# Kernel tuning notes

Measured on AMD Instinct MI355X. Metric: run time of the kernel, lower is better.

Reference implementation:

```python
import jax, jax.numpy as jnp
import numpy as np

B = 16
H_DIM = 512
N_HEADS = 8
HEAD_DIM = H_DIM // N_HEADS  # 64
EPS = 1e-5
DST_LENS = 256 + 16 * np.arange(B)  # ragged dst sizes, total 6016
SRC_LENS = 512 - 8 * np.arange(B)   # ragged src sizes, total 7232


def _pad_info(lens):
    # gather/scatter indices to move between flat ragged layout and [B, Lmax, D]
    lens = np.asarray(lens)
    off = np.concatenate([[0], np.cumsum(lens)[:-1]])
    gid = np.repeat(np.arange(len(lens)), lens)
    pos = np.arange(int(lens.sum())) - np.repeat(off, lens)
    Lmax = int(lens.max())
    mask = jnp.asarray(np.arange(Lmax)[None, :] < lens[:, None])
    return gid, pos, Lmax, mask


def _bn(x, g, b):
    # BatchNorm1d forward with batch statistics (training-mode normalization)
    m = x.mean(0)
    v = ((x - m) ** 2).mean(0)
    return (x - m) / jnp.sqrt(v + EPS) * g + b


def setup_inputs() -> dict:
    key = jax.random.key(0)
    ks = jax.random.split(key, 20)
    total_src = int(SRC_LENS.sum())
    total_dst = int(DST_LENS.sum())
    w = lambda k, shape: jax.random.normal(k, shape, jnp.float32) * 0.02
    return {
        "src_h": jax.random.normal(ks[0], (total_src, H_DIM), jnp.float32),
        "dst_h": jax.random.normal(ks[1], (total_dst, H_DIM), jnp.float32),
        "src_num_verts": jnp.asarray(SRC_LENS, jnp.int32),
        "dst_num_verts": jnp.asarray(DST_LENS, jnp.int32),
        "Wq": w(ks[2], (H_DIM, H_DIM)), "bq": w(ks[3], (H_DIM,)),
        "Wk": w(ks[4], (H_DIM, H_DIM)), "bk": w(ks[5], (H_DIM,)),
        "Wv": w(ks[6], (H_DIM, H_DIM)), "bv": w(ks[7], (H_DIM,)),
        "Wm": w(ks[8], (H_DIM, H_DIM)), "bm": w(ks[9], (H_DIM,)),
        "W1": w(ks[10], (H_DIM, 2 * H_DIM)), "b1": w(ks[11], (H_DIM,)),
        "g1": jnp.ones((H_DIM,), jnp.float32), "be1": jnp.zeros((H_DIM,), jnp.float32),
        "W2": w(ks[12], (H_DIM, H_DIM)), "b2": w(ks[13], (H_DIM,)),
        "g2": jnp.ones((H_DIM,), jnp.float32), "be2": jnp.zeros((H_DIM,), jnp.float32),
    }


def reference(src_h, dst_h, src_num_verts, dst_num_verts,
              Wq, bq, Wk, bk, Wv, bv, Wm, bm,
              W1, b1, g1, be1, W2, b2, g2, be2):
    s_lens = np.asarray(src_num_verts)
    d_lens = np.asarray(dst_num_verts)
    sg, sp, Ls, smask = _pad_info(s_lens)
    dg, dp, Ld, dmask = _pad_info(d_lens)

    # ragged -> padded [B, L, D]
    src_pad = jnp.zeros((B, Ls, H_DIM), src_h.dtype).at[sg, sp].set(src_h)
    dst_pad = jnp.zeros((B, Ld, H_DIM), dst_h.dtype).at[dg, dp].set(dst_h)

    # Conv1d(k=1) projections; channel c = d*num_heads + h -> reshape (head_dim, n_heads)
    q = (dst_pad @ Wq.T + bq).reshape(B, Ld, HEAD_DIM, N_HEADS)
    k = (src_pad @ Wk.T + bk).reshape(B, Ls, HEAD_DIM, N_HEADS)
    v = (src_pad @ Wv.T + bv).reshape(B, Ls, HEAD_DIM, N_HEADS)

    scores = jnp.einsum('bndh,bmdh->bhnm', q, k) / 8.0  # sqrt(head_dim)=8
    scores = jnp.where(smask[:, None, None, :], scores, -1e9)
    attn = jax.nn.softmax(scores, axis=-1)
    o = jnp.einsum('bhnm,bmdh->bndh', attn, v).reshape(B, Ld, H_DIM)
    o = o @ Wm.T + bm  # merge Conv1d(k=1)

    # padded -> ragged
    h_msg = o[dg, dp]  # [total_dst, h_dim]

    h = dst_h
    x = jnp.concatenate([h, h_msg], axis=-1)
    x = _bn(x @ W1.T + b1, g1, be1)
    x = jax.nn.relu(x)
    x = _bn(x @ W2.T + b2, g2, be2)
    return h + x
```

## Files before the change

### kernel.cpp

```cpp
#include <hip/hip_runtime.h>
#include <hip/hip_bf16.h>

#define H_DIM 512
#define N_HEADS 8
#define HEAD_DIM 64
#define NBATCH 16

typedef __attribute__((ext_vector_type(8))) short short8;
typedef __attribute__((ext_vector_type(4))) float floatx4;

typedef unsigned short us16;

#define SW3(r) ((((r) >> 1) & 3) | (((r) & 1) << 2))

#define PERMC(c) ((((c) & 7) << 6) | ((c) >> 3))
#define IPERMC(cp) ((((cp) & 63) << 3) | ((cp) >> 6))

__device__ inline unsigned short f2bf(float f) {
  unsigned int u = __float_as_uint(f);
  unsigned int r = (u + 0x7fffu + ((u >> 16) & 1u)) >> 16;
  return (unsigned short)r;
}

__device__ inline void gld16(const us16* g, us16* l) {
  __builtin_amdgcn_global_load_lds(
      (const __attribute__((address_space(1))) void*)g,
      (__attribute__((address_space(3))) void*)l, 16, 0, 0);
}

__global__ __launch_bounds__(256) void prep_all(
    const float* __restrict__ src_h, const float* __restrict__ dst_h,
    const float* __restrict__ Wq, const float* __restrict__ Wk,
    const float* __restrict__ Wv, const float* __restrict__ W1,
    const float* __restrict__ W2, const float* __restrict__ Wm,
    const float* __restrict__ b1, const float* __restrict__ bm,
    us16* __restrict__ src_bf, us16* __restrict__ dst_bf,
    us16* __restrict__ Wqb, us16* __restrict__ Wkv, us16* __restrict__ Wf,
    us16* __restrict__ W2b, float* __restrict__ b1p, float* __restrict__ st,
    int n_src, int n_dst) {
  __shared__ __align__(16) us16 As[64 * 48];
  __shared__ __align__(16) us16 Bs[64 * 48];
  const int blk = blockIdx.x;
  const int t = threadIdx.x;

  if (blk < 2048) {
    if (blk == 0) {
      float4 z = make_float4(0.f, 0.f, 0.f, 0.f);
      ((float4*)st)[t] = z;
      ((float4*)st)[t + 256] = z;
    }
    const float* srcs[7] = {src_h, dst_h, Wq, Wk, Wv, W1, W2};
    us16* dsts[7] = {src_bf, dst_bf, Wqb, Wkv, Wkv + 262144, Wf, W2b};
    int ns[7] = {n_src, n_dst, 262144, 262144, 262144, 262144, 262144};
    const int md_[7] = {0, 0, 2, 2, 0, 1, 0};
    for (int rg = 0; rg < 7; ++rg) {
      const float* sp = srcs[rg];
      us16* dp = dsts[rg];
      const int mode = md_[rg];
      for (int i = (blk * 256 + t) * 4; i < ns[rg]; i += 2048 * 256 * 4) {
        int js, jd;
        if (mode == 1) {
          js = ((i >> 9) * 1024) + (i & 511);
          jd = js;
        } else if (mode == 2) {
          int r = i >> 9;
          js = i;
          jd = (PERMC(r) << 9) + (i & 511);
        } else {
          js = i; jd = i;
        }
        float4 v = *(const float4*)(sp + js);
        ushort4 o;
        o.x = f2bf(v.x); o.y = f2bf(v.y); o.z = f2bf(v.z); o.w = f2bf(v.w);
        *(ushort4*)(dp + jd) = o;
      }
    }
  } else if (blk < 2112) {
    const int bx = (blk - 2048) & 7, byk = (blk - 2048) >> 3;
    const int w = t >> 6, lane = t & 63;
    const int lane15 = lane & 15, quad = lane >> 4;
    const int wm = w >> 1, wn = w & 1;
    const int bn_ = bx * 64, bk = byk * 64;
    floatx4 acc[2][2];
#pragma unroll
    for (int a = 0; a < 2; ++a)
#pragma unroll
      for (int c = 0; c < 2; ++c) acc[a][c] = (floatx4){0.f, 0.f, 0.f, 0.f};
    for (int j0 = 0; j0 < 512; j0 += 32) {
      {
        int n = t >> 2, jj0 = (t & 3) * 8;
        const float* rp = W1 + (size_t)(bn_ + n) * 1024 + 512 + j0 + jj0;
        float4 va = *(const float4*)(rp);
        float4 vb = *(const float4*)(rp + 4);
        ushort4 pa, pb;
        pa.x = f2bf(va.x); pa.y = f2bf(va.y); pa.z = f2bf(va.z); pa.w = f2bf(va.w);
        pb.x = f2bf(vb.x); pb.y = f2bf(vb.y); pb.z = f2bf(vb.z); pb.w = f2bf(vb.w);
        *(ushort4*)(As + n * 48 + jj0) = pa;
        *(ushort4*)(As + n * 48 + jj0 + 4) = pb;
      }
      {
        int jj = t >> 3, kc0 = (t & 7) * 8;
        const float* rp = Wm + (size_t)(j0 + jj) * 512 + bk + kc0;
        float4 va = *(const float4*)(rp);
        float4 vb = *(const float4*)(rp + 4);
        float vv[8] = {va.x, va.y, va.z, va.w, vb.x, vb.y, vb.z, vb.w};
#pragma unroll
        for (int e = 0; e < 8; ++e) Bs[(kc0 + e) * 48 + jj] = f2bf(vv[e]);
      }
      __syncthreads();
      short8 a_[2], b_[2];
#pragma unroll
      for (int mt = 0; mt < 2; ++mt)
        a_[mt] = *(const short8*)(As + (wm * 32 + mt * 16 + lane15) * 48 + quad * 8);
#pragma unroll
      for (int nt = 0; nt < 2; ++nt)
        b_[nt] = *(const short8*)(Bs + (wn * 32 + nt * 16 + lane15) * 48 + quad * 8);
#pragma unroll
      for (int mt = 0; mt < 2; ++mt)
#pragma unroll
        for (int nt = 0; nt < 2; ++nt)
          acc[mt][nt] = __builtin_amdgcn_mfma_f32_16x16x32_bf16(
              a_[mt], b_[nt], acc[mt][nt], 0, 0, 0);
      __syncthreads();
    }
#pragma unroll
    for (int mt = 0; mt < 2; ++mt) {
      int n0 = bn_ + wm * 32 + mt * 16 + quad * 4;
#pragma unroll
      for (int nt = 0; nt < 2; ++nt) {
        int k = bk + wn * 32 + nt * 16 + lane15;
        int kp = PERMC(k);
#pragma unroll
        for (int r = 0; r < 4; ++r)
          Wf[(size_t)(n0 + r) * 1024 + 512 + kp] = f2bf(acc[mt][nt][r]);
      }
    }
  } else {
    int n = (blk - 2112) * 256 + t;
    if (n < 512) {
      const float* rp = W1 + (size_t)n * 1024 + 512;
      float s = 0.f;
      for (int j = 0; j < 512; j += 4) {
        float4 a = *(const float4*)(rp + j);
        float4 c = *(const float4*)(bm + j);
        s += a.x * c.x + a.y * c.y + a.z * c.z + a.w * c.w;
      }
      b1p[n] = b1[n] + s;
    }
  }
}

__device__ inline void gemm_body(
    const us16* __restrict__ A1, const us16* __restrict__ A2,
    const us16* __restrict__ W,
    const float* __restrict__ bias0, const float* __restrict__ bias1,
    void* __restrict__ C0, void* __restrict__ C1, float* __restrict__ stats,
    int M, int N, int K, int mode, int bx, int by) {
  __shared__ __align__(16) us16 As[2 * 64 * 64];
  __shared__ __align__(16) us16 Bs[2 * 128 * 64];
  const int t = threadIdx.x, w = t >> 6, lane = t & 63;
  const int lane15 = lane & 15, quad = lane >> 4;
  const int bm = bx * 64, bn = by * 128;
  const int lrow = lane >> 3;
  const int sl = lane & 7;

  floatx4 acc[4][2];
#pragma unroll
  for (int a = 0; a < 4; ++a)
#pragma unroll
    for (int c = 0; c < 2; ++c) acc[a][c] = (floatx4){0.f, 0.f, 0.f, 0.f};

  const int nk = K >> 6;

#define ISSUE(i, b)                                                          \
  {                                                                          \
    int k0 = (i) << 6;                                                       \
    const us16* Ab = (k0 < 512) ? A1 : A2;                                   \
    int ka = k0 & 511;                                                       \
    _Pragma("unroll")                                                        \
    for (int p = 0; p < 2; ++p) {                                            \
      int rbase = p * 32 + w * 8;                                            \
      int row = rbase + lrow;                                                \
      int kg = sl ^ SW3(row);                                                \
      gld16(Ab + (size_t)(bm + row) * 512 + ka + kg * 8,                     \
            As + (b) * 4096 + rbase * 64);                                   \
    }                                                                        \
    _Pragma("unroll")                                                        \
    for (int p = 0; p < 4; ++p) {                                            \
      int rbase = p * 32 + w * 8;                                            \
      int row = rbase + lrow;                                                \
      int kg = sl ^ SW3(row);                                                \
      gld16(W + (size_t)(bn + row) * K + k0 + kg * 8,                        \
            Bs + (b) * 8192 + rbase * 64);                                   \
    }                                                                        \
  }

  ISSUE(0, 0);
  if (nk > 1) ISSUE(1, 1);
  for (int i = 0; i < nk; ++i) {
    const int cur = i & 1;
    if (i + 1 < nk) {
      asm volatile("s_waitcnt vmcnt(6)" ::: "memory");
    } else {
      asm volatile("s_waitcnt vmcnt(0)" ::: "memory");
    }
    __builtin_amdgcn_s_barrier();
    asm volatile("" ::: "memory");
#pragma unroll
    for (int kh = 0; kh < 2; ++kh) {
      const int g = kh * 4 + quad;
      short8 a_[4], b_[2];
#pragma unroll
      for (int mt = 0; mt < 4; ++mt) {
        int r = mt * 16 + lane15;
        a_[mt] = *(const short8*)(As + cur * 4096 + r * 64 + (g ^ SW3(r)) * 8);
      }
#pragma unroll
      for (int nt = 0; nt < 2; ++nt) {
        int c = w * 32 + nt * 16 + lane15;
        b_[nt] = *(const short8*)(Bs + cur * 8192 + c * 64 + (g ^ SW3(c)) * 8);
      }
#pragma unroll
      for (int mt = 0; mt < 4; ++mt)
#pragma unroll
        for (int nt = 0; nt < 2; ++nt)
          acc[mt][nt] = __builtin_amdgcn_mfma_f32_16x16x32_bf16(
              a_[mt], b_[nt], acc[mt][nt], 0, 0, 0);
    }
    asm volatile("" ::: "memory");
    __builtin_amdgcn_s_barrier();
    asm volatile("" ::: "memory");
    if (i + 2 < nk) ISSUE(i + 2, cur);
  }
#undef ISSUE

  if (mode == 0) {
#pragma unroll
    for (int nt = 0; nt < 2; ++nt) {
      int col = bn + w * 32 + nt * 16 + lane15;
      float bv = bias0[col];
      float s = 0.f, qq = 0.f;
#pragma unroll
      for (int mt = 0; mt < 4; ++mt) {
        int row0 = bm + mt * 16 + quad * 4;
#pragma unroll
        for (int r = 0; r < 4; ++r) {
          float val = acc[mt][nt][r] + bv;
          ((float*)C0)[(size_t)(row0 + r) * N + col] = val;
          s += val; qq = fmaf(val, val, qq);
        }
      }
      s += __shfl_xor(s, 16); s += __shfl_xor(s, 32);
      qq += __shfl_xor(qq, 16); qq += __shfl_xor(qq, 32);
      if (quad == 0) {
        atomicAdd(&stats[col], s);
        atomicAdd(&stats[512 + col], qq);
      }
    }
  } else if (mode == 1) {
#pragma unroll
    for (int nt = 0; nt < 2; ++nt) {
      int col = bn + w * 32 + nt * 16 + lane15;
      float bv = bias0[IPERMC(col)];
#pragma unroll
      for (int mt = 0; mt < 4; ++mt) {
        int row0 = bm + mt * 16 + quad * 4;
#pragma unroll
        for (int r = 0; r < 4; ++r)
          ((us16*)C0)[(size_t)(row0 + r) * 512 + col] = f2bf(acc[mt][nt][r] + bv);
      }
    }
  } else {
#pragma unroll
    for (int nt = 0; nt < 2; ++nt) {
      int col = bn + w * 32 + nt * 16 + lane15;
      if (col < 512) {
        float bv = bias0[IPERMC(col)];
#pragma unroll
        for (int mt = 0; mt < 4; ++mt) {
          int row0 = bm + mt * 16 + quad * 4;
#pragma unroll
          for (int r = 0; r < 4; ++r)
            ((us16*)C0)[(size_t)(row0 + r) * 512 + col] = f2bf(acc[mt][nt][r] + bv);
        }
      } else {
        int cv = col - 512;
        float bv = bias1[cv];
        int plane = (cv & 7) * 64 + (cv >> 3);
#pragma unroll
        for (int mt = 0; mt < 4; ++mt) {
          int row0 = bm + mt * 16 + quad * 4;
          ushort4 pk;
          pk.x = f2bf(acc[mt][nt][0] + bv);
          pk.y = f2bf(acc[mt][nt][1] + bv);
          pk.z = f2bf(acc[mt][nt][2] + bv);
          pk.w = f2bf(acc[mt][nt][3] + bv);
          *(ushort4*)((us16*)C1 + (size_t)plane * M + row0) = pk;
        }
      }
    }
  }
}

__global__ __launch_bounds__(256) void gemm_ffn(
    const us16* __restrict__ A1, const us16* __restrict__ A2,
    const us16* __restrict__ W,
    const float* __restrict__ bias0, void* __restrict__ C0,
    float* __restrict__ stats, int M, int K) {
  int b = blockIdx.x;
  int i = (b & 7) * ((int)gridDim.x >> 3) + (b >> 3);
  gemm_body(A1, A2, W, bias0, nullptr, C0, nullptr, stats, M, 512, K, 0,
            i >> 2, i & 3);
}

__global__ __launch_bounds__(256) void gemm_qkv(
    const us16* __restrict__ dst_bf, const us16* __restrict__ src_bf,
    const us16* __restrict__ Wqb, const us16* __restrict__ Wkv,
    const float* __restrict__ bq, const float* __restrict__ bk,
    const float* __restrict__ bv,
    us16* __restrict__ Qh, us16* __restrict__ Kh, us16* __restrict__ Vt,
    int Md, int Ms) {
  int b = blockIdx.x;
  int i = (b & 7) * ((int)gridDim.x >> 3) + (b >> 3);
  int nq = (Md / 64) * 4;
  if (i < nq) {
    gemm_body(dst_bf, dst_bf, Wqb, bq, nullptr, Qh, nullptr, nullptr,
              Md, 512, 512, 1, i >> 2, i & 3);
  } else {
    int j = i - nq;
    gemm_body(src_bf, src_bf, Wkv, bk, bv, Kh, Vt, nullptr,
              Ms, 1024, 512, 4, j >> 3, j & 7);
  }
}

__global__ __launch_bounds__(256) void attn_v6(
    const us16* __restrict__ Qh, const us16* __restrict__ Kh,
    const us16* __restrict__ Vt, const int* __restrict__ dlens,
    const int* __restrict__ slens, us16* __restrict__ O,
    int Md, int Ms) {
  const int b = blockIdx.x, h = blockIdx.y, tile = blockIdx.z;
  int doff = 0, soff = 0;
  for (int i = 0; i < NBATCH; ++i)
    if (i < b) { doff += dlens[i]; soff += slens[i]; }
  const int dlen = dlens[b], slen = slens[b];
  if (tile * 64 >= dlen) return;

  __shared__ __align__(16) us16 Ks[2 * 64 * 64];
  __shared__ __align__(16) us16 Vts[2 * 64 * 64];
  __shared__ __align__(16) us16 Pw[4][16 * 72];

  const int t = threadIdx.x, wv = t >> 6, lane = t & 63;
  const int lane15 = lane & 15, quad = lane >> 4;
  const int i0w = tile * 64 + wv * 16;
  const bool active = i0w < dlen;

  const us16* Qp = Qh + ((size_t)(doff + (active ? i0w : 0))) * 512 + h * 64;
  const us16* Kp = Kh + ((size_t)soff) * 512 + h * 64;
  const us16* Vtp = Vt + ((size_t)h * 64) * Ms + soff;

  short8 af0 = *(const short8*)(Qp + (size_t)lane15 * 512 + quad * 8);
  short8 af1 = *(const short8*)(Qp + (size_t)lane15 * 512 + 32 + quad * 8);

  floatx4 oa[4];
#pragma unroll
  for (int nt = 0; nt < 4; ++nt) oa[nt] = (floatx4){0.f, 0.f, 0.f, 0.f};
  float m_r[4] = {-3.0e38f, -3.0e38f, -3.0e38f, -3.0e38f};
  float l_r[4] = {0.f, 0.f, 0.f, 0.f};

  const int nc = (slen + 63) >> 6;

#define KVST(c, bu)                                                       \
  {                                                                       \
    int jb = (c) << 6;                                                    \
    _Pragma("unroll")                                                     \
    for (int p = 0; p < 2; ++p) {                                         \
      int row = wv * 16 + p * 8 + (lane >> 3);                            \
      int slt = lane & 7;                                                 \
      int kg = slt ^ SW3(row);                                            \
      gld16(Kp + (size_t)(jb + row) * 512 + kg * 8,                       \
            Ks + (bu) * 4096 + (wv * 16 + p * 8) * 64);                   \
      gld16(Vtp + (size_t)row * Ms + jb + kg * 8,                         \
            Vts + (bu) * 4096 + (wv * 16 + p * 8) * 64);                  \
    }                                                                     \
  }

  KVST(0, 0);
  if (nc > 1) KVST(1, 1);
  for (int c = 0; c < nc; ++c) {
    const int cur = c & 1;
    if (c + 1 < nc) {
      asm volatile("s_waitcnt vmcnt(4)" ::: "memory");
    } else {
      asm volatile("s_waitcnt vmcnt(0)" ::: "memory");
    }
    __builtin_amdgcn_s_barrier();
    asm volatile("" ::: "memory");

    if (active) {
      const int j0 = c << 6;
      floatx4 s[4];
#pragma unroll
      for (int jt = 0; jt < 4; ++jt) {
        int j = jt * 16 + lane15;
        short8 b0 = *(const short8*)(Ks + cur * 4096 + j * 64 + ((quad ^ SW3(j)) * 8));
        short8 b1 = *(const short8*)(Ks + cur * 4096 + j * 64 + (((4 + quad) ^ SW3(j)) * 8));
        floatx4 a = (floatx4){0.f, 0.f, 0.f, 0.f};
        a = __builtin_amdgcn_mfma_f32_16x16x32_bf16(af0, b0, a, 0, 0, 0);
        a = __builtin_amdgcn_mfma_f32_16x16x32_bf16(af1, b1, a, 0, 0, 0);
        s[jt] = a;
      }
      float mx[4] = {-3.0e38f, -3.0e38f, -3.0e38f, -3.0e38f};
#pragma unroll
      for (int jt = 0; jt < 4; ++jt) {
        bool valid = (j0 + jt * 16 + lane15) < slen;
#pragma unroll
        for (int r = 0; r < 4; ++r) {
          float v = valid ? s[jt][r] * 0.125f : -3.0e38f;
          s[jt][r] = v;
          mx[r] = fmaxf(mx[r], v);
        }
      }
#pragma unroll
      for (int r = 0; r < 4; ++r) {
        mx[r] = fmaxf(mx[r], __shfl_xor(mx[r], 1));
        mx[r] = fmaxf(mx[r], __shfl_xor(mx[r], 2));
        mx[r] = fmaxf(mx[r], __shfl_xor(mx[r], 4));
        mx[r] = fmaxf(mx[r], __shfl_xor(mx[r], 8));
      }
      float al[4], sum[4];
#pragma unroll
      for (int r = 0; r < 4; ++r) {
        float mn = fmaxf(m_r[r], mx[r]);
        al[r] = __expf(m_r[r] - mn);
        m_r[r] = mn;
        sum[r] = 0.f;
      }
#pragma unroll
      for (int jt = 0; jt < 4; ++jt)
#pragma unroll
        for (int r = 0; r < 4; ++r) {
          float e = __expf(s[jt][r] - m_r[r]);
          sum[r] += e;
          Pw[wv][(quad * 4 + r) * 72 + jt * 16 + lane15] = f2bf(e);
        }
#pragma unroll
      for (int r = 0; r < 4; ++r) {
        sum[r] += __shfl_xor(sum[r], 1);
        sum[r] += __shfl_xor(sum[r], 2);
        sum[r] += __shfl_xor(sum[r], 4);
        sum[r] += __shfl_xor(sum[r], 8);
        l_r[r] = l_r[r] * al[r] + sum[r];
      }
#pragma unroll
      for (int nt = 0; nt < 4; ++nt)
#pragma unroll
        for (int r = 0; r < 4; ++r) oa[nt][r] *= al[r];
      short8 pa0 = *(const short8*)(&Pw[wv][lane15 * 72 + quad * 8]);
      short8 pa1 = *(const short8*)(&Pw[wv][lane15 * 72 + 32 + quad * 8]);
#pragma unroll
      for (int nt = 0; nt < 4; ++nt) {
        int d = nt * 16 + lane15;
        short8 v0 = *(const short8*)(Vts + cur * 4096 + d * 64 + ((quad ^ SW3(d)) * 8));
        short8 v1 = *(const short8*)(Vts + cur * 4096 + d * 64 + (((4 + quad) ^ SW3(d)) * 8));
        oa[nt] = __builtin_amdgcn_mfma_f32_16x16x32_bf16(pa0, v0, oa[nt], 0, 0, 0);
        oa[nt] = __builtin_amdgcn_mfma_f32_16x16x32_bf16(pa1, v1, oa[nt], 0, 0, 0);
      }
    }

    asm volatile("" ::: "memory");
    __builtin_amdgcn_s_barrier();
    asm volatile("" ::: "memory");
    if (c + 2 < nc) KVST(c + 2, cur);
  }
#undef KVST

  if (active) {
    float linv[4];
#pragma unroll
    for (int r = 0; r < 4; ++r) linv[r] = 1.f / l_r[r];
#pragma unroll
    for (int r = 0; r < 4; ++r) {
      int i = quad * 4 + r;
      us16* orow = O + (size_t)(doff + i0w + i) * H_DIM + h * 64;
#pragma unroll
      for (int nt = 0; nt < 4; ++nt) {
        int d = nt * 16 + lane15;
        orow[d] = f2bf(oa[nt][r] * linv[r]);
      }
    }
  }
}

__global__ __launch_bounds__(256) void bn_apply(
    const float* __restrict__ X, const float* __restrict__ stats,
    const float* __restrict__ g, const float* __restrict__ be,
    const float* __restrict__ resid, void* __restrict__ Y,
    int M, float invM, int relu, int out_bf) {
  const size_t total = (size_t)M * H_DIM;
  for (size_t i = (size_t)blockIdx.x * 256 + threadIdx.x; i < total;
       i += (size_t)gridDim.x * 256) {
    int c = (int)(i & (H_DIM - 1));
    float mean = stats[c] * invM;
    float var = fmaf(-mean, mean, stats[H_DIM + c] * invM);
    float x = X[i];
    float y = (x - mean) * rsqrtf(var + 1e-5f) * g[c] + be[c];
    if (relu) y = fmaxf(y, 0.f);
    if (resid) y += resid[i];
    if (out_bf) ((us16*)Y)[i] = f2bf(y);
    else ((float*)Y)[i] = y;
  }
}

extern "C" void kernel_launch(void* const* d_in, const int* in_sizes, int n_in,
                              void* d_out, int out_size, void* d_ws, size_t ws_size,
                              hipStream_t stream) {
  const float* src_h = (const float*)d_in[0];
  const float* dst_h = (const float*)d_in[1];
  const int* s_lens  = (const int*)d_in[2];
  const int* d_lens  = (const int*)d_in[3];
  const float* Wq = (const float*)d_in[4];  const float* bq = (const float*)d_in[5];
  const float* Wk = (const float*)d_in[6];  const float* bk = (const float*)d_in[7];
  const float* Wv = (const float*)d_in[8];  const float* bv = (const float*)d_in[9];
  const float* Wm = (const float*)d_in[10]; const float* bm = (const float*)d_in[11];
  const float* W1 = (const float*)d_in[12]; const float* b1 = (const float*)d_in[13];
  const float* g1 = (const float*)d_in[14]; const float* be1 = (const float*)d_in[15];
  const float* W2 = (const float*)d_in[16]; const float* b2 = (const float*)d_in[17];
  const float* g2 = (const float*)d_in[18]; const float* be2 = (const float*)d_in[19];

  const int total_src = in_sizes[0] / H_DIM;
  const int total_dst = in_sizes[1] / H_DIM;

  char* ws = (char*)d_ws;
  us16* src_bf = (us16*)(ws + 0);
  us16* dst_bf = (us16*)(ws + 7405568);
  us16* wbf    = (us16*)(ws + 13565952);
  float* b1p   = (float*)(ws + 16711680);
  us16* Qh     = (us16*)(ws + 17235968);
  us16* Kh     = (us16*)(ws + 23396352);
  us16* Vt     = (us16*)(ws + 30801920);
  us16* Ob     = (us16*)(ws + 38207488);
  us16* X1bf   = (us16*)(ws + 44367872);
  float* st    = (float*)(ws + 50528256);
  float* X1    = (float*)(ws + 17235968);
  float* X2    = (float*)(ws + 30801920);
  float* st1 = st, *st2 = st + 1024;

  us16* Wqb = wbf;
  us16* Wkv = wbf + 262144;
  us16* Wf  = wbf + 786432;
  us16* W2b = wbf + 1310720;

  const int mbd = total_dst / 64;
  const int mbs = total_src / 64;
  const dim3 blk256(256);

  prep_all<<<dim3(2114), blk256, 0, stream>>>(
      src_h, dst_h, Wq, Wk, Wv, W1, W2, Wm, b1, bm,
      src_bf, dst_bf, Wqb, Wkv, Wf, W2b, b1p, st,
      total_src * H_DIM, total_dst * H_DIM);

  gemm_qkv<<<dim3(mbd * 4 + mbs * 8), blk256, 0, stream>>>(
      dst_bf, src_bf, Wqb, Wkv, bq, bk, bv, Qh, Kh, Vt, total_dst, total_src);

  attn_v6<<<dim3(NBATCH, N_HEADS, 8), blk256, 0, stream>>>(
      Qh, Kh, Vt, d_lens, s_lens, Ob, total_dst, total_src);

  gemm_ffn<<<dim3(mbd * 4), blk256, 0, stream>>>(
      dst_bf, Ob, Wf, b1p, X1, st1, total_dst, 1024);

  bn_apply<<<dim3(512), blk256, 0, stream>>>(X1, st1, g1, be1, nullptr, X1bf,
                                             total_dst, 1.f / (float)total_dst, 1, 1);

  gemm_ffn<<<dim3(mbd * 4), blk256, 0, stream>>>(
      X1bf, X1bf, W2b, b2, X2, st2, total_dst, 512);

  bn_apply<<<dim3(512), blk256, 0, stream>>>(X2, st2, g2, be2, dst_h, d_out,
                                             total_dst, 1.f / (float)total_dst, 0, 0);
}
```

Before: 237.1 us.

## Use 128x128 tiles for the QKV projection GEMM with remainder-aware XCD mapping

Adds a separate GEMM body for the Q/K/V projections that uses a 128x128 output tile with a 2x2 wave layout, instead of 64x128. Each block reuses every loaded A and W tile across four times as many MFMAs, cutting global and LDS traffic per flop and halving the number of blocks. The source row count is not a multiple of 128, so stores in the last tile are guarded, but its loads still read past the end of the source buffer. The block-to-XCD remapping now handles grid sizes that are not divisible by 8. The FFN GEMM path is cleaned up into a single-mode body.

```diff
diff --git a/kernel.cpp b/kernel.cpp
--- a/kernel.cpp
+++ b/kernel.cpp
@@ -153,9 +153,8 @@
 __device__ inline void gemm_body(
     const us16* __restrict__ A1, const us16* __restrict__ A2,
     const us16* __restrict__ W,
-    const float* __restrict__ bias0, const float* __restrict__ bias1,
-    void* __restrict__ C0, void* __restrict__ C1, float* __restrict__ stats,
-    int M, int N, int K, int mode, int bx, int by) {
+    const float* __restrict__ bias0, void* __restrict__ C0,
+    float* __restrict__ stats, int M, int N, int K, int bx, int by) {
   __shared__ __align__(16) us16 As[2 * 64 * 64];
   __shared__ __align__(16) us16 Bs[2 * 128 * 64];
   const int t = threadIdx.x, w = t >> 6, lane = t & 63;
@@ -234,37 +233,120 @@
   }
 #undef ISSUE
 
-  if (mode == 0) {
-#pragma unroll
-    for (int nt = 0; nt < 2; ++nt) {
-      int col = bn + w * 32 + nt * 16 + lane15;
-      float bv = bias0[col];
-      float s = 0.f, qq = 0.f;
+#pragma unroll
+  for (int nt = 0; nt < 2; ++nt) {
+    int col = bn + w * 32 + nt * 16 + lane15;
+    float bv = bias0[col];
+    float s = 0.f, qq = 0.f;
+#pragma unroll
+    for (int mt = 0; mt < 4; ++mt) {
+      int row0 = bm + mt * 16 + quad * 4;
+#pragma unroll
+      for (int r = 0; r < 4; ++r) {
+        float val = acc[mt][nt][r] + bv;
+        ((float*)C0)[(size_t)(row0 + r) * N + col] = val;
+        s += val; qq = fmaf(val, val, qq);
+      }
+    }
+    s += __shfl_xor(s, 16); s += __shfl_xor(s, 32);
+    qq += __shfl_xor(qq, 16); qq += __shfl_xor(qq, 32);
+    if (quad == 0) {
+      atomicAdd(&stats[col], s);
+      atomicAdd(&stats[512 + col], qq);
+    }
+  }
+}
+
+__device__ inline void gemm128_body(
+    const us16* __restrict__ A, const us16* __restrict__ W,
+    const float* __restrict__ bias0, const float* __restrict__ bias1,
+    void* __restrict__ C0, void* __restrict__ C1,
+    int M, int mode, int bx, int by) {
+  __shared__ __align__(16) us16 As[2 * 128 * 64];
+  __shared__ __align__(16) us16 Bs[2 * 128 * 64];
+  const int t = threadIdx.x, w = t >> 6, lane = t & 63;
+  const int lane15 = lane & 15, quad = lane >> 4;
+  const int wm = w >> 1, wn = w & 1;
+  const int bm = bx * 128, bn = by * 128;
+  const int lrow = lane >> 3;
+  const int sl = lane & 7;
+
+  floatx4 acc[4][4];
+#pragma unroll
+  for (int a = 0; a < 4; ++a)
+#pragma unroll
+    for (int c = 0; c < 4; ++c) acc[a][c] = (floatx4){0.f, 0.f, 0.f, 0.f};
+
+  const int nk = 8;
+
+#define ISSUE8(i, b)                                                         \
+  {                                                                          \
+    int k0 = (i) << 6;                                                       \
+    _Pragma("unroll")                                                        \
+    for (int p = 0; p < 4; ++p) {                                            \
+      int rbase = p * 32 + w * 8;                                            \
+      int row = rbase + lrow;                                                \
+      int kg = sl ^ SW3(row);                                                \
+      gld16(A + (size_t)(bm + row) * 512 + k0 + kg * 8,                      \
+            As + (b) * 8192 + rbase * 64);                                   \
+    }                                                                        \
+    _Pragma("unroll")                                                        \
+    for (int p = 0; p < 4; ++p) {                                            \
+      int rbase = p * 32 + w * 8;                                            \
+      int row = rbase + lrow;                                                \
+      int kg = sl ^ SW3(row);                                                \
+      gld16(W + (size_t)(bn + row) * 512 + k0 + kg * 8,                      \
+            Bs + (b) * 8192 + rbase * 64);                                   \
+    }                                                                        \
+  }
+
+  ISSUE8(0, 0);
+  ISSUE8(1, 1);
+  for (int i = 0; i < nk; ++i) {
+    const int cur = i & 1;
+    if (i + 1 < nk) {
+      asm volatile("s_waitcnt vmcnt(8)" ::: "memory");
+    } else {
+      asm volatile("s_waitcnt vmcnt(0)" ::: "memory");
+    }
+    __builtin_amdgcn_s_barrier();
+    asm volatile("" ::: "memory");
+#pragma unroll
+    for (int kh = 0; kh < 2; ++kh) {
+      const int g = kh * 4 + quad;
+      short8 a_[4], b_[4];
 #pragma unroll
       for (int mt = 0; mt < 4; ++mt) {
-        int row0 = bm + mt * 16 + quad * 4;
-#pragma unroll
-        for (int r = 0; r < 4; ++r) {
-          float val = acc[mt][nt][r] + bv;
-          ((float*)C0)[(size_t)(row0 + r) * N + col] = val;
-          s += val; qq = fmaf(val, val, qq);
-        }
-      }
-      s += __shfl_xor(s, 16); s += __shfl_xor(s, 32);
-      qq += __shfl_xor(qq, 16); qq += __shfl_xor(qq, 32);
-      if (quad == 0) {
-        atomicAdd(&stats[col], s);
-        atomicAdd(&stats[512 + col], qq);
-      }
-    }
-  } else if (mode == 1) {
-#pragma unroll
-    for (int nt = 0; nt < 2; ++nt) {
-      int col = bn + w * 32 + nt * 16 + lane15;
+        int r = wm * 64 + mt * 16 + lane15;
+        a_[mt] = *(const short8*)(As + cur * 8192 + r * 64 + (g ^ SW3(r)) * 8);
+      }
+#pragma unroll
+      for (int nt = 0; nt < 4; ++nt) {
+        int c = wn * 64 + nt * 16 + lane15;
+        b_[nt] = *(const short8*)(Bs + cur * 8192 + c * 64 + (g ^ SW3(c)) * 8);
+      }
+#pragma unroll
+      for (int mt = 0; mt < 4; ++mt)
+#pragma unroll
+        for (int nt = 0; nt < 4; ++nt)
+          acc[mt][nt] = __builtin_amdgcn_mfma_f32_16x16x32_bf16(
+              a_[mt], b_[nt], acc[mt][nt], 0, 0, 0);
+    }
+    asm volatile("" ::: "memory");
+    __builtin_amdgcn_s_barrier();
+    asm volatile("" ::: "memory");
+    if (i + 2 < nk) ISSUE8(i + 2, cur);
+  }
+#undef ISSUE8
+
+  if (mode == 1) {
+#pragma unroll
+    for (int nt = 0; nt < 4; ++nt) {
+      int col = bn + wn * 64 + nt * 16 + lane15;
       float bv = bias0[IPERMC(col)];
 #pragma unroll
       for (int mt = 0; mt < 4; ++mt) {
-        int row0 = bm + mt * 16 + quad * 4;
+        int row0 = bm + wm * 64 + mt * 16 + quad * 4;
 #pragma unroll
         for (int r = 0; r < 4; ++r)
           ((us16*)C0)[(size_t)(row0 + r) * 512 + col] = f2bf(acc[mt][nt][r] + bv);
@@ -272,16 +354,18 @@
     }
   } else {
 #pragma unroll
-    for (int nt = 0; nt < 2; ++nt) {
-      int col = bn + w * 32 + nt * 16 + lane15;
+    for (int nt = 0; nt < 4; ++nt) {
+      int col = bn + wn * 64 + nt * 16 + lane15;
       if (col < 512) {
         float bv = bias0[IPERMC(col)];
 #pragma unroll
         for (int mt = 0; mt < 4; ++mt) {
-          int row0 = bm + mt * 16 + quad * 4;
-#pragma unroll
-          for (int r = 0; r < 4; ++r)
-            ((us16*)C0)[(size_t)(row0 + r) * 512 + col] = f2bf(acc[mt][nt][r] + bv);
+          int row0 = bm + wm * 64 + mt * 16 + quad * 4;
+          if (row0 < M) {
+#pragma unroll
+            for (int r = 0; r < 4; ++r)
+              ((us16*)C0)[(size_t)(row0 + r) * 512 + col] = f2bf(acc[mt][nt][r] + bv);
+          }
         }
       } else {
         int cv = col - 512;
@@ -289,13 +373,15 @@
         int plane = (cv & 7) * 64 + (cv >> 3);
 #pragma unroll
         for (int mt = 0; mt < 4; ++mt) {
-          int row0 = bm + mt * 16 + quad * 4;
-          ushort4 pk;
-          pk.x = f2bf(acc[mt][nt][0] + bv);
-          pk.y = f2bf(acc[mt][nt][1] + bv);
-          pk.z = f2bf(acc[mt][nt][2] + bv);
-          pk.w = f2bf(acc[mt][nt][3] + bv);
-          *(ushort4*)((us16*)C1 + (size_t)plane * M + row0) = pk;
+          int row0 = bm + wm * 64 + mt * 16 + quad * 4;
+          if (row0 < M) {
+            ushort4 pk;
+            pk.x = f2bf(acc[mt][nt][0] + bv);
+            pk.y = f2bf(acc[mt][nt][1] + bv);
+            pk.z = f2bf(acc[mt][nt][2] + bv);
+            pk.w = f2bf(acc[mt][nt][3] + bv);
+            *(ushort4*)((us16*)C1 + (size_t)plane * M + row0) = pk;
+          }
         }
       }
     }
@@ -309,8 +395,7 @@
     float* __restrict__ stats, int M, int K) {
   int b = blockIdx.x;
   int i = (b & 7) * ((int)gridDim.x >> 3) + (b >> 3);
-  gemm_body(A1, A2, W, bias0, nullptr, C0, nullptr, stats, M, 512, K, 0,
-            i >> 2, i & 3);
+  gemm_body(A1, A2, W, bias0, C0, stats, M, 512, K, i >> 2, i & 3);
 }
 
 __global__ __launch_bounds__(256) void gemm_qkv(
@@ -321,15 +406,16 @@
     us16* __restrict__ Qh, us16* __restrict__ Kh, us16* __restrict__ Vt,
     int Md, int Ms) {
   int b = blockIdx.x;
-  int i = (b & 7) * ((int)gridDim.x >> 3) + (b >> 3);
-  int nq = (Md / 64) * 4;
+  int nwg = (int)gridDim.x;
+  int q = nwg >> 3, r = nwg & 7;
+  int xcd = b & 7, pos = b >> 3;
+  int i = (xcd < r ? xcd * (q + 1) : r * (q + 1) + (xcd - r) * q) + pos;
+  int nq = (Md / 128) * 4;
   if (i < nq) {
-    gemm_body(dst_bf, dst_bf, Wqb, bq, nullptr, Qh, nullptr, nullptr,
-              Md, 512, 512, 1, i >> 2, i & 3);
+    gemm128_body(dst_bf, Wqb, bq, nullptr, Qh, nullptr, Md, 1, i >> 2, i & 3);
   } else {
     int j = i - nq;
-    gemm_body(src_bf, src_bf, Wkv, bk, bv, Kh, Vt, nullptr,
-              Ms, 1024, 512, 4, j >> 3, j & 7);
+    gemm128_body(src_bf, Wkv, bk, bv, Kh, Vt, Ms, 4, j >> 3, j & 7);
   }
 }
 
@@ -551,7 +637,8 @@
   us16* W2b = wbf + 1310720;
 
   const int mbd = total_dst / 64;
-  const int mbs = total_src / 64;
+  const int mbd128 = total_dst / 128;
+  const int mbs128 = (total_src + 127) / 128;
   const dim3 blk256(256);
 
   prep_all<<<dim3(2114), blk256, 0, stream>>>(
@@ -559,7 +646,7 @@
       src_bf, dst_bf, Wqb, Wkv, Wf, W2b, b1p, st,
       total_src * H_DIM, total_dst * H_DIM);
 
-  gemm_qkv<<<dim3(mbd * 4 + mbs * 8), blk256, 0, stream>>>(
+  gemm_qkv<<<dim3(mbd128 * 4 + mbs128 * 8), blk256, 0, stream>>>(
       dst_bf, src_bf, Wqb, Wkv, bq, bk, bv, Qh, Kh, Vt, total_dst, total_src);
 
   attn_v6<<<dim3(NBATCH, N_HEADS, 8), blk256, 0, stream>>>(
```

Result: slower. 244.6 us (+3.2%).

## Fuse FFN GEMMs and batchnorm passes into one cooperative kernel with grid syncs

Applied to the files above, without the earlier changes.

Replaces the two FFN GEMM launches and two batchnorm-apply launches with a single cooperative kernel. The kernel runs GEMM1, grid sync, BN1+ReLU on its own tile, grid sync, GEMM2, grid sync, then BN2+residual. It falls back to separate launches if the cooperative launch fails. This removes three launch gaps and part of the BN traffic, since each block normalizes only its own tile. In exchange it adds grid-wide barriers and needs all 376 blocks to be resident at once.

```diff
diff --git a/kernel.cpp b/kernel.cpp
--- a/kernel.cpp
+++ b/kernel.cpp
@@ -1,5 +1,8 @@
 #include <hip/hip_runtime.h>
 #include <hip/hip_bf16.h>
+#include <hip/hip_cooperative_groups.h>
+
+namespace cg = cooperative_groups;
 
 #define H_DIM 512
 #define N_HEADS 8
@@ -151,13 +154,12 @@
 }
 
 __device__ inline void gemm_body(
+    us16* As, us16* Bs,
     const us16* __restrict__ A1, const us16* __restrict__ A2,
     const us16* __restrict__ W,
     const float* __restrict__ bias0, const float* __restrict__ bias1,
     void* __restrict__ C0, void* __restrict__ C1, float* __restrict__ stats,
     int M, int N, int K, int mode, int bx, int by) {
-  __shared__ __align__(16) us16 As[2 * 64 * 64];
-  __shared__ __align__(16) us16 Bs[2 * 128 * 64];
   const int t = threadIdx.x, w = t >> 6, lane = t & 63;
   const int lane15 = lane & 15, quad = lane >> 4;
   const int bm = bx * 64, bn = by * 128;
@@ -302,17 +304,6 @@
   }
 }
 
-__global__ __launch_bounds__(256) void gemm_ffn(
-    const us16* __restrict__ A1, const us16* __restrict__ A2,
-    const us16* __restrict__ W,
-    const float* __restrict__ bias0, void* __restrict__ C0,
-    float* __restrict__ stats, int M, int K) {
-  int b = blockIdx.x;
-  int i = (b & 7) * ((int)gridDim.x >> 3) + (b >> 3);
-  gemm_body(A1, A2, W, bias0, nullptr, C0, nullptr, stats, M, 512, K, 0,
-            i >> 2, i & 3);
-}
-
 __global__ __launch_bounds__(256) void gemm_qkv(
     const us16* __restrict__ dst_bf, const us16* __restrict__ src_bf,
     const us16* __restrict__ Wqb, const us16* __restrict__ Wkv,
@@ -320,175 +311,32 @@
     const float* __restrict__ bv,
     us16* __restrict__ Qh, us16* __restrict__ Kh, us16* __restrict__ Vt,
     int Md, int Ms) {
+  __shared__ __align__(16) us16 As[2 * 64 * 64];
+  __shared__ __align__(16) us16 Bs[2 * 128 * 64];
   int b = blockIdx.x;
   int i = (b & 7) * ((int)gridDim.x >> 3) + (b >> 3);
   int nq = (Md / 64) * 4;
   if (i < nq) {
-    gemm_body(dst_bf, dst_bf, Wqb, bq, nullptr, Qh, nullptr, nullptr,
+    gemm_body(As, Bs, dst_bf, dst_bf, Wqb, bq, nullptr, Qh, nullptr, nullptr,
               Md, 512, 512, 1, i >> 2, i & 3);
   } else {
     int j = i - nq;
-    gemm_body(src_bf, src_bf, Wkv, bk, bv, Kh, Vt, nullptr,
+    gemm_body(As, Bs, src_bf, src_bf, Wkv, bk, bv, Kh, Vt, nullptr,
               Ms, 1024, 512, 4, j >> 3, j & 7);
   }
 }
 
-__global__ __launch_bounds__(256) void attn_v6(
-    const us16* __restrict__ Qh, const us16* __restrict__ Kh,
-    const us16* __restrict__ Vt, const int* __restrict__ dlens,
-    const int* __restrict__ slens, us16* __restrict__ O,
-    int Md, int Ms) {
-  const int b = blockIdx.x, h = blockIdx.y, tile = blockIdx.z;
-  int doff = 0, soff = 0;
-  for (int i = 0; i < NBATCH; ++i)
-    if (i < b) { doff += dlens[i]; soff += slens[i]; }
-  const int dlen = dlens[b], slen = slens[b];
-  if (tile * 64 >= dlen) return;
-
-  __shared__ __align__(16) us16 Ks[2 * 64 * 64];
-  __shared__ __align__(16) us16 Vts[2 * 64 * 64];
-  __shared__ __align__(16) us16 Pw[4][16 * 72];
-
-  const int t = threadIdx.x, wv = t >> 6, lane = t & 63;
-  const int lane15 = lane & 15, quad = lane >> 4;
-  const int i0w = tile * 64 + wv * 16;
-  const bool active = i0w < dlen;
-
-  const us16* Qp = Qh + ((size_t)(doff + (active ? i0w : 0))) * 512 + h * 64;
-  const us16* Kp = Kh + ((size_t)soff) * 512 + h * 64;
-  const us16* Vtp = Vt + ((size_t)h * 64) * Ms + soff;
-
-  short8 af0 = *(const short8*)(Qp + (size_t)lane15 * 512 + quad * 8);
-  short8 af1 = *(const short8*)(Qp + (size_t)lane15 * 512 + 32 + quad * 8);
-
-  floatx4 oa[4];
-#pragma unroll
-  for (int nt = 0; nt < 4; ++nt) oa[nt] = (floatx4){0.f, 0.f, 0.f, 0.f};
-  float m_r[4] = {-3.0e38f, -3.0e38f, -3.0e38f, -3.0e38f};
-  float l_r[4] = {0.f, 0.f, 0.f, 0.f};
-
-  const int nc = (slen + 63) >> 6;
-
-#define KVST(c, bu)                                                       \
-  {                                                                       \
-    int jb = (c) << 6;                                                    \
-    _Pragma("unroll")                                                     \
-    for (int p = 0; p < 2; ++p) {                                         \
-      int row = wv * 16 + p * 8 + (lane >> 3);                            \
-      int slt = lane & 7;                                                 \
-      int kg = slt ^ SW3(row);                                            \
-      gld16(Kp + (size_t)(jb + row) * 512 + kg * 8,                       \
-            Ks + (bu) * 4096 + (wv * 16 + p * 8) * 64);                   \
-      gld16(Vtp + (size_t)row * Ms + jb + kg * 8,                         \
-            Vts + (bu) * 4096 + (wv * 16 + p * 8) * 64);                  \
-    }                                                                     \
-  }
-
-  KVST(0, 0);
-  if (nc > 1) KVST(1, 1);
-  for (int c = 0; c < nc; ++c) {
-    const int cur = c & 1;
-    if (c + 1 < nc) {
-      asm volatile("s_waitcnt vmcnt(4)" ::: "memory");
-    } else {
-      asm volatile("s_waitcnt vmcnt(0)" ::: "memory");
-    }
-    __builtin_amdgcn_s_barrier();
-    asm volatile("" ::: "memory");
-
-    if (active) {
-      const int j0 = c << 6;
-      floatx4 s[4];
-#pragma unroll
-      for (int jt = 0; jt < 4; ++jt) {
-        int j = jt * 16 + lane15;
-        short8 b0 = *(const short8*)(Ks + cur * 4096 + j * 64 + ((quad ^ SW3(j)) * 8));
-        short8 b1 = *(const short8*)(Ks + cur * 4096 + j * 64 + (((4 + quad) ^ SW3(j)) * 8));
-        floatx4 a = (floatx4){0.f, 0.f, 0.f, 0.f};
-        a = __builtin_amdgcn_mfma_f32_16x16x32_bf16(af0, b0, a, 0, 0, 0);
-        a = __builtin_amdgcn_mfma_f32_16x16x32_bf16(af1, b1, a, 0, 0, 0);
-        s[jt] = a;
-      }
-      float mx[4] = {-3.0e38f, -3.0e38f, -3.0e38f, -3.0e38f};
-#pragma unroll
-      for (int jt = 0; jt < 4; ++jt) {
-        bool valid = (j0 + jt * 16 + lane15) < slen;
-#pragma unroll
-        for (int r = 0; r < 4; ++r) {
-          float v = valid ? s[jt][r] * 0.125f : -3.0e38f;
-          s[jt][r] = v;
-          mx[r] = fmaxf(mx[r], v);
-        }
-      }
-#pragma unroll
-      for (int r = 0; r < 4; ++r) {
-        mx[r] = fmaxf(mx[r], __shfl_xor(mx[r], 1));
-        mx[r] = fmaxf(mx[r], __shfl_xor(mx[r], 2));
-        mx[r] = fmaxf(mx[r], __shfl_xor(mx[r], 4));
-        mx[r] = fmaxf(mx[r], __shfl_xor(mx[r], 8));
-      }
-      float al[4], sum[4];
-#pragma unroll
-      for (int r = 0; r < 4; ++r) {
-        float mn = fmaxf(m_r[r], mx[r]);
-        al[r] = __expf(m_r[r] - mn);
-        m_r[r] = mn;
-        sum[r] = 0.f;
-      }
-#pragma unroll
-      for (int jt = 0; jt < 4; ++jt)
-#pragma unroll
-        for (int r = 0; r < 4; ++r) {
-          float e = __expf(s[jt][r] - m_r[r]);
-          sum[r] += e;
-          Pw[wv][(quad * 4 + r) * 72 + jt * 16 + lane15] = f2bf(e);
-        }
-#pragma unroll
-      for (int r = 0; r < 4; ++r) {
-        sum[r] += __shfl_xor(sum[r], 1);
-        sum[r] += __shfl_xor(sum[r], 2);
-        sum[r] += __shfl_xor(sum[r], 4);
-        sum[r] += __shfl_xor(sum[r], 8);
-        l_r[r] = l_r[r] * al[r] + sum[r];
-      }
-#pragma unroll
-      for (int nt = 0; nt < 4; ++nt)
-#pragma unroll
-        for (int r = 0; r < 4; ++r) oa[nt][r] *= al[r];
-      short8 pa0 = *(const short8*)(&Pw[wv][lane15 * 72 + quad * 8]);
-      short8 pa1 = *(const short8*)(&Pw[wv][lane15 * 72 + 32 + quad * 8]);
-#pragma unroll
-      for (int nt = 0; nt < 4; ++nt) {
-        int d = nt * 16 + lane15;
-        short8 v0 = *(const short8*)(Vts + cur * 4096 + d * 64 + ((quad ^ SW3(d)) * 8));
-        short8 v1 = *(const short8*)(Vts + cur * 4096 + d * 64 + (((4 + quad) ^ SW3(d)) * 8));
-        oa[nt] = __builtin_amdgcn_mfma_f32_16x16x32_bf16(pa0, v0, oa[nt], 0, 0, 0);
-        oa[nt] = __builtin_amdgcn_mfma_f32_16x16x32_bf16(pa1, v1, oa[nt], 0, 0, 0);
-      }
-    }
-
-    asm volatile("" ::: "memory");
-    __builtin_amdgcn_s_barrier();
-    asm volatile("" ::: "memory");
-    if (c + 2 < nc) KVST(c + 2, cur);
-  }
-#undef KVST
-
-  if (active) {
-    float linv[4];
-#pragma unroll
-    for (int r = 0; r < 4; ++r) linv[r] = 1.f / l_r[r];
-#pragma unroll
-    for (int r = 0; r < 4; ++r) {
-      int i = quad * 4 + r;
-      us16* orow = O + (size_t)(doff + i0w + i) * H_DIM + h * 64;
-#pragma unroll
-      for (int nt = 0; nt < 4; ++nt) {
-        int d = nt * 16 + lane15;
-        orow[d] = f2bf(oa[nt][r] * linv[r]);
-      }
-    }
-  }
+__global__ __launch_bounds__(256) void gemm_ffn(
+    const us16* __restrict__ A1, const us16* __restrict__ A2,
+    const us16* __restrict__ W,
+    const float* __restrict__ bias0, void* __restrict__ C0,
+    float* __restrict__ stats, int M, int K) {
+  __shared__ __align__(16) us16 As[2 * 64 * 64];
+  __shared__ __align__(16) us16 Bs[2 * 128 * 64];
+  int b = blockIdx.x;
+  int i = (b & 7) * ((int)gridDim.x >> 3) + (b >> 3);
+  gemm_body(As, Bs, A1, A2, W, bias0, nullptr, C0, nullptr, stats,
+            M, 512, K, 0, i >> 2, i & 3);
 }
 
 __global__ __launch_bounds__(256) void bn_apply(
@@ -511,6 +359,249 @@
   }
 }
 
+__global__ __launch_bounds__(256) void fused_tail(
+    const us16* __restrict__ dst_bf, const us16* __restrict__ Ob,
+    const us16* __restrict__ Wf, const us16* __restrict__ W2b,
+    const float* __restrict__ b1p, const float* __restrict__ b2,
+    const float* __restrict__ g1, const float* __restrict__ be1,
+    const float* __restrict__ g2, const float* __restrict__ be2,
+    const float* __restrict__ dst_h,
+    float* __restrict__ X1, us16* __restrict__ X1bf, float* __restrict__ X2,
+    float* __restrict__ out, float* __restrict__ st, int M) {
+  __shared__ __align__(16) us16 As[2 * 64 * 64];
+  __shared__ __align__(16) us16 Bs[2 * 128 * 64];
+  cg::grid_group grid = cg::this_grid();
+  const int b = blockIdx.x;
+  const int nblk = (int)gridDim.x;
+  const int i = (b & 7) * (nblk >> 3) + (b >> 3);
+  const int bx = i >> 2, by = i & 3;
+  const int t = threadIdx.x;
+  const float invM = 1.f / (float)M;
+
+  gemm_body(As, Bs, dst_bf, Ob, Wf, b1p, nullptr, X1, nullptr, st,
+            M, 512, 1024, 0, bx, by);
+  grid.sync();
+
+  {
+    float* sl = (float*)As;
+    float* tl = sl + 128;
+    const int c0 = by * 128;
+    if (t < 128) {
+      int c = c0 + t;
+      float mean = st[c] * invM;
+      float var = fmaf(-mean, mean, st[512 + c] * invM);
+      float inv = rsqrtf(var + 1e-5f) * g1[c];
+      sl[t] = inv;
+      tl[t] = be1[c] - mean * inv;
+    }
+    __syncthreads();
+    const float* Xs = X1 + (size_t)(bx * 64) * 512 + c0;
+    us16* Yd = X1bf + (size_t)(bx * 64) * 512 + c0;
+    for (int j = t * 4; j < 64 * 128; j += 1024) {
+      int row = j >> 7, col = j & 127;
+      float4 v = *(const float4*)(Xs + (size_t)row * 512 + col);
+      ushort4 o;
+      o.x = f2bf(fmaxf(fmaf(v.x, sl[col], tl[col]), 0.f));
+      o.y = f2bf(fmaxf(fmaf(v.y, sl[col + 1], tl[col + 1]), 0.f));
+      o.z = f2bf(fmaxf(fmaf(v.z, sl[col + 2], tl[col + 2]), 0.f));
+      o.w = f2bf(fmaxf(fmaf(v.w, sl[col + 3], tl[col + 3]), 0.f));
+      *(ushort4*)(Yd + (size_t)row * 512 + col) = o;
+    }
+  }
+  grid.sync();
+
+  gemm_body(As, Bs, X1bf, X1bf, W2b, b2, nullptr, X2, nullptr, st + 1024,
+            M, 512, 512, 0, bx, by);
+  grid.sync();
+
+  {
+    float* sl = (float*)As;
+    float* tl = sl + 128;
+    const int c0 = by * 128;
+    if (t < 128) {
+      int c = c0 + t;
+      float mean = st[1024 + c] * invM;
+      float var = fmaf(-mean, mean, st[1536 + c] * invM);
+      float inv = rsqrtf(var + 1e-5f) * g2[c];
+      sl[t] = inv;
+      tl[t] = be2[c] - mean * inv;
+    }
+    __syncthreads();
+    const float* Xs = X2 + (size_t)(bx * 64) * 512 + c0;
+    const float* Rs = dst_h + (size_t)(bx * 64) * 512 + c0;
+    float* Yd = out + (size_t)(bx * 64) * 512 + c0;
+    for (int j = t * 4; j < 64 * 128; j += 1024) {
+      int row = j >> 7, col = j & 127;
+      float4 v = *(const float4*)(Xs + (size_t)row * 512 + col);
+      float4 rr = *(const float4*)(Rs + (size_t)row * 512 + col);
+      float4 o;
+      o.x = fmaf(v.x, sl[col], tl[col]) + rr.x;
+      o.y = fmaf(v.y, sl[col + 1], tl[col + 1]) + rr.y;
+      o.z = fmaf(v.z, sl[col + 2], tl[col + 2]) + rr.z;
+      o.w = fmaf(v.w, sl[col + 3], tl[col + 3]) + rr.w;
+      *(float4*)(Yd + (size_t)row * 512 + col) = o;
+    }
+  }
+}
+
+__global__ __launch_bounds__(256) void attn_v6(
+    const us16* __restrict__ Qh, const us16* __restrict__ Kh,
+    const us16* __restrict__ Vt, const int* __restrict__ dlens,
+    const int* __restrict__ slens, us16* __restrict__ O,
+    int Md, int Ms) {
+  const int b = blockIdx.x, h = blockIdx.y, tile = blockIdx.z;
+  int doff = 0, soff = 0;
+  for (int i = 0; i < NBATCH; ++i)
+    if (i < b) { doff += dlens[i]; soff += slens[i]; }
+  const int dlen = dlens[b], slen = slens[b];
+  if (tile * 64 >= dlen) return;
+
+  __shared__ __align__(16) us16 Ks[2 * 64 * 64];
+  __shared__ __align__(16) us16 Vts[2 * 64 * 64];
+  __shared__ __align__(16) us16 Pw[4][16 * 72];
+
+  const int t = threadIdx.x, wv = t >> 6, lane = t & 63;
+  const int lane15 = lane & 15, quad = lane >> 4;
+  const int i0w = tile * 64 + wv * 16;
+  const bool active = i0w < dlen;
+
+  const us16* Qp = Qh + ((size_t)(doff + (active ? i0w : 0))) * 512 + h * 64;
+  const us16* Kp = Kh + ((size_t)soff) * 512 + h * 64;
+  const us16* Vtp = Vt + ((size_t)h * 64) * Ms + soff;
+
+  short8 af0 = *(const short8*)(Qp + (size_t)lane15 * 512 + quad * 8);
+  short8 af1 = *(const short8*)(Qp + (size_t)lane15 * 512 + 32 + quad * 8);
+
+  floatx4 oa[4];
+#pragma unroll
+  for (int nt = 0; nt < 4; ++nt) oa[nt] = (floatx4){0.f, 0.f, 0.f, 0.f};
+  float m_r[4] = {-3.0e38f, -3.0e38f, -3.0e38f, -3.0e38f};
+  float l_r[4] = {0.f, 0.f, 0.f, 0.f};
+
+  const int nc = (slen + 63) >> 6;
+
+#define KVST(c, bu)                                                       \
+  {                                                                       \
+    int jb = (c) << 6;                                                    \
+    _Pragma("unroll")                                                     \
+    for (int p = 0; p < 2; ++p) {                                         \
+      int row = wv * 16 + p * 8 + (lane >> 3);                            \
+      int slt = lane & 7;                                                 \
+      int kg = slt ^ SW3(row);                                            \
+      gld16(Kp + (size_t)(jb + row) * 512 + kg * 8,                       \
+            Ks + (bu) * 4096 + (wv * 16 + p * 8) * 64);                   \
+      gld16(Vtp + (size_t)row * Ms + jb + kg * 8,                         \
+            Vts + (bu) * 4096 + (wv * 16 + p * 8) * 64);                  \
+    }                                                                     \
+  }
+
+  KVST(0, 0);
+  if (nc > 1) KVST(1, 1);
+  for (int c = 0; c < nc; ++c) {
+    const int cur = c & 1;
+    if (c + 1 < nc) {
+      asm volatile("s_waitcnt vmcnt(4)" ::: "memory");
+    } else {
+      asm volatile("s_waitcnt vmcnt(0)" ::: "memory");
+    }
+    __builtin_amdgcn_s_barrier();
+    asm volatile("" ::: "memory");
+
+    if (active) {
+      const int j0 = c << 6;
+      floatx4 s[4];
+#pragma unroll
+      for (int jt = 0; jt < 4; ++jt) {
+        int j = jt * 16 + lane15;
+        short8 b0 = *(const short8*)(Ks + cur * 4096 + j * 64 + ((quad ^ SW3(j)) * 8));
+        short8 b1 = *(const short8*)(Ks + cur * 4096 + j * 64 + (((4 + quad) ^ SW3(j)) * 8));
+        floatx4 a = (floatx4){0.f, 0.f, 0.f, 0.f};
+        a = __builtin_amdgcn_mfma_f32_16x16x32_bf16(af0, b0, a, 0, 0, 0);
+        a = __builtin_amdgcn_mfma_f32_16x16x32_bf16(af1, b1, a, 0, 0, 0);
+        s[jt] = a;
+      }
+      float mx[4] = {-3.0e38f, -3.0e38f, -3.0e38f, -3.0e38f};
+#pragma unroll
+      for (int jt = 0; jt < 4; ++jt) {
+        bool valid = (j0 + jt * 16 + lane15) < slen;
+#pragma unroll
+        for (int r = 0; r < 4; ++r) {
+          float v = valid ? s[jt][r] * 0.125f : -3.0e38f;
+          s[jt][r] = v;
+          mx[r] = fmaxf(mx[r], v);
+        }
+      }
+#pragma unroll
+      for (int r = 0; r < 4; ++r) {
+        mx[r] = fmaxf(mx[r], __shfl_xor(mx[r], 1));
+        mx[r] = fmaxf(mx[r], __shfl_xor(mx[r], 2));
+        mx[r] = fmaxf(mx[r], __shfl_xor(mx[r], 4));
+        mx[r] = fmaxf(mx[r], __shfl_xor(mx[r], 8));
+      }
+      float al[4], sum[4];
+#pragma unroll
+      for (int r = 0; r < 4; ++r) {
+        float mn = fmaxf(m_r[r], mx[r]);
+        al[r] = __expf(m_r[r] - mn);
+        m_r[r] = mn;
+        sum[r] = 0.f;
+      }
+#pragma unroll
+      for (int jt = 0; jt < 4; ++jt)
+#pragma unroll
+        for (int r = 0; r < 4; ++r) {
+          float e = __expf(s[jt][r] - m_r[r]);
+          sum[r] += e;
+          Pw[wv][(quad * 4 + r) * 72 + jt * 16 + lane15] = f2bf(e);
+        }
+#pragma unroll
+      for (int r = 0; r < 4; ++r) {
+        sum[r] += __shfl_xor(sum[r], 1);
+        sum[r] += __shfl_xor(sum[r], 2);
+        sum[r] += __shfl_xor(sum[r], 4);
+        sum[r] += __shfl_xor(sum[r], 8);
+        l_r[r] = l_r[r] * al[r] + sum[r];
+      }
+#pragma unroll
+      for (int nt = 0; nt < 4; ++nt)
+#pragma unroll
+        for (int r = 0; r < 4; ++r) oa[nt][r] *= al[r];
+      short8 pa0 = *(const short8*)(&Pw[wv][lane15 * 72 + quad * 8]);
+      short8 pa1 = *(const short8*)(&Pw[wv][lane15 * 72 + 32 + quad * 8]);
+#pragma unroll
+      for (int nt = 0; nt < 4; ++nt) {
+        int d = nt * 16 + lane15;
+        short8 v0 = *(const short8*)(Vts + cur * 4096 + d * 64 + ((quad ^ SW3(d)) * 8));
+        short8 v1 = *(const short8*)(Vts + cur * 4096 + d * 64 + (((4 + quad) ^ SW3(d)) * 8));
+        oa[nt] = __builtin_amdgcn_mfma_f32_16x16x32_bf16(pa0, v0, oa[nt], 0, 0, 0);
+        oa[nt] = __builtin_amdgcn_mfma_f32_16x16x32_bf16(pa1, v1, oa[nt], 0, 0, 0);
+      }
+    }
+
+    asm volatile("" ::: "memory");
+    __builtin_amdgcn_s_barrier();
+    asm volatile("" ::: "memory");
+    if (c + 2 < nc) KVST(c + 2, cur);
+  }
+#undef KVST
+
+  if (active) {
+    float linv[4];
+#pragma unroll
+    for (int r = 0; r < 4; ++r) linv[r] = 1.f / l_r[r];
+#pragma unroll
+    for (int r = 0; r < 4; ++r) {
+      int i = quad * 4 + r;
+      us16* orow = O + (size_t)(doff + i0w + i) * H_DIM + h * 64;
+#pragma unroll
+      for (int nt = 0; nt < 4; ++nt) {
+        int d = nt * 16 + lane15;
+        orow[d] = f2bf(oa[nt][r] * linv[r]);
+      }
+    }
+  }
+}
+
 extern "C" void kernel_launch(void* const* d_in, const int* in_sizes, int n_in,
                               void* d_out, int out_size, void* d_ws, size_t ws_size,
                               hipStream_t stream) {
@@ -565,15 +656,32 @@
   attn_v6<<<dim3(NBATCH, N_HEADS, 8), blk256, 0, stream>>>(
       Qh, Kh, Vt, d_lens, s_lens, Ob, total_dst, total_src);
 
-  gemm_ffn<<<dim3(mbd * 4), blk256, 0, stream>>>(
-      dst_bf, Ob, Wf, b1p, X1, st1, total_dst, 1024);
-
-  bn_apply<<<dim3(512), blk256, 0, stream>>>(X1, st1, g1, be1, nullptr, X1bf,
-                                             total_dst, 1.f / (float)total_dst, 1, 1);
-
-  gemm_ffn<<<dim3(mbd * 4), blk256, 0, stream>>>(
-      X1bf, X1bf, W2b, b2, X2, st2, total_dst, 512);
-
-  bn_apply<<<dim3(512), blk256, 0, stream>>>(X2, st2, g2, be2, dst_h, d_out,
-                                             total_dst, 1.f / (float)total_dst, 0, 0);
-}
+  {
+    const us16* a_dst = dst_bf; const us16* a_ob = Ob;
+    const us16* a_wf = Wf; const us16* a_w2 = W2b;
+    const float* a_b1p = b1p; const float* a_b2 = b2;
+    const float* a_g1 = g1; const float* a_be1 = be1;
+    const float* a_g2 = g2; const float* a_be2 = be2;
+    const float* a_dh = dst_h;
+    float* a_x1 = X1; us16* a_x1bf = X1bf; float* a_x2 = X2;
+    float* a_out = (float*)d_out; float* a_st = st;
+    int a_m = total_dst;
+    void* args[] = {&a_dst, &a_ob, &a_wf, &a_w2, &a_b1p, &a_b2,
+                    &a_g1, &a_be1, &a_g2, &a_be2, &a_dh,
+                    &a_x1, &a_x1bf, &a_x2, &a_out, &a_st, &a_m};
+    hipError_t err = hipLaunchCooperativeKernel(
+        (const void*)fused_tail, dim3(mbd * 4), blk256, args, 0, stream);
+    if (err != hipSuccess) {
+      gemm_ffn<<<dim3(mbd * 4), blk256, 0, stream>>>(
+          dst_bf, Ob, Wf, b1p, X1, st1, total_dst, 1024);
+      bn_apply<<<dim3(512), blk256, 0, stream>>>(
+          X1, st1, g1, be1, nullptr, X1bf, total_dst,
+          1.f / (float)total_dst, 1, 1);
+      gemm_ffn<<<dim3(mbd * 4), blk256, 0, stream>>>(
+          X1bf, X1bf, W2b, b2, X2, st2, total_dst, 512);
+      bn_apply<<<dim3(512), blk256, 0, stream>>>(
+          X2, st2, g2, be2, dst_h, d_out, total_dst,
+          1.f / (float)total_dst, 0, 0);
+    }
+  }
+}
```

Result: slower. 399.8 us (+68.6%).
